# Kernel optimization log

Hardware: AMD Instinct MI355X
Metric: run time of the kernel (lower is better)

Reference implementation:

```python
import jax, jax.numpy as jnp
import numpy as np

B, T, D, H = 4, 1024, 1024, 16
NUM_BUCKETS = 320
MAX_DIST = 800
LN_EPS = 1e-5


def _rel_bucket(T):
    # bidirectional T5-style relative position buckets
    ctx = jnp.arange(T)[:, None]
    mem = jnp.arange(T)[None, :]
    rel = mem - ctx  # (T, T)
    half = NUM_BUCKETS // 2  # 160
    bucket = (rel > 0).astype(jnp.int32) * half
    n = jnp.abs(rel)
    max_exact = half // 2  # 80
    is_small = n < max_exact
    n_f = jnp.maximum(n, 1).astype(jnp.float32)
    large = max_exact + (
        jnp.log(n_f / max_exact) / np.log(MAX_DIST / max_exact) * (half - max_exact)
    ).astype(jnp.int32)
    large = jnp.minimum(large, half - 1)
    return bucket + jnp.where(is_small, n, large)


def setup_inputs() -> dict:
    key = jax.random.key(0)
    ks = jax.random.split(key, 12)
    s = 0.02
    return {
        "x": jax.random.normal(ks[0], (B, T, D), jnp.float32),
        "ln_w": jnp.ones((D,), jnp.float32),
        "ln_b": jnp.zeros((D,), jnp.float32),
        "wq": jax.random.normal(ks[1], (D, D), jnp.float32) * s,
        "bq": jnp.zeros((D,), jnp.float32),
        "wk": jax.random.normal(ks[2], (D, D), jnp.float32) * s,
        "bk": jnp.zeros((D,), jnp.float32),
        "wv": jax.random.normal(ks[3], (D, D), jnp.float32) * s,
        "bv": jnp.zeros((D,), jnp.float32),
        "wo": jax.random.normal(ks[4], (D, D), jnp.float32) * s,
        "bo": jnp.zeros((D,), jnp.float32),
        "rel_emb": jax.random.normal(ks[5], (NUM_BUCKETS, H), jnp.float32) * s,
        "grep_w": jax.random.normal(ks[6], (8, D // H), jnp.float32) * s,
        "grep_b": jnp.zeros((8,), jnp.float32),
        "grep_a": jnp.ones((1, H, 1, 1), jnp.float32),
    }


def reference(x, ln_w, ln_b, wq, bq, wk, bk, wv, bv, wo, bo, rel_emb, grep_w, grep_b, grep_a):
    Bb, Tt, Dd = x.shape
    hd = Dd // H
    scaling = hd ** -0.5
    # pre-norm LayerNorm
    mu = jnp.mean(x, -1, keepdims=True)
    var = jnp.mean((x - mu) ** 2, -1, keepdims=True)
    h = (x - mu) / jnp.sqrt(var + LN_EPS) * ln_w + ln_b
    # projections (q pre-scaled as in fairseq/WavLM)
    q = (h @ wq.T + bq) * scaling
    k = h @ wk.T + bk
    v = h @ wv.T + bv
    q = q.reshape(Bb, Tt, H, hd).transpose(0, 2, 1, 3)  # (B,H,T,hd)
    k = k.reshape(Bb, Tt, H, hd).transpose(0, 2, 1, 3)
    v = v.reshape(Bb, Tt, H, hd).transpose(0, 2, 1, 3)
    # bucketed relative position bias: (H, T, T)
    buckets = _rel_bucket(Tt)
    pos_bias = rel_emb[buckets].transpose(2, 0, 1)
    # gru_rel_pos gating (per batch, head, query position)
    alpha = 32.0
    ql = q * (alpha / scaling)  # undo scaling, multiply by alpha
    g = jax.nn.sigmoid((ql @ grep_w.T + grep_b).reshape(Bb, H, Tt, 2, 4).sum(-1))
    gate_a, gate_b = g[..., 0:1], g[..., 1:2]  # (B,H,T,1)
    gate = gate_a * (gate_b * grep_a - 1.0) + 2.0
    # attention
    scores = jnp.einsum('bhtd,bhsd->bhts', q, k) + gate * pos_bias[None]
    attn = jax.nn.softmax(scores, axis=-1)
    out = jnp.einsum('bhts,bhsd->bhtd', attn, v).transpose(0, 2, 1, 3).reshape(Bb, Tt, Dd)
    # output projection, dropout (identity in eval), residual
    out = out @ wo.T + bo + x
    pos_bias_out = jnp.broadcast_to(pos_bias[None], (Bb, H, Tt, Tt)).reshape(Bb * H, Tt, Tt)
    return out, pos_bias_out
```

## Files before the change

### kernel.cpp

```cpp
#include <hip/hip_runtime.h>

typedef unsigned short u16;
typedef __attribute__((ext_vector_type(8))) short short8;
typedef __attribute__((ext_vector_type(4))) short short4v;
typedef __attribute__((ext_vector_type(4))) float floatx4;

#define MFMA16(a, b, c) __builtin_amdgcn_mfma_f32_16x16x32_bf16(a, b, c, 0, 0, 0)

__device__ __forceinline__ float bf2f(u16 u) {
  return __uint_as_float(((unsigned int)u) << 16);
}
__device__ __forceinline__ u16 f2bf(float f) {
  unsigned int u = __float_as_uint(f);
  unsigned int r = (u + 0x7fffu + ((u >> 16) & 1u)) >> 16;
  return (u16)r;
}
__device__ __forceinline__ void gl_lds16(const u16* g, u16* lds_wave_base) {
  __builtin_amdgcn_global_load_lds(
      (const __attribute__((address_space(1))) unsigned int*)g,
      (__attribute__((address_space(3))) unsigned int*)lds_wave_base, 16, 0, 0);
}

__global__ __launch_bounds__(256) void ln_kernel(
    const float* __restrict__ x, const float* __restrict__ w, const float* __restrict__ bb,
    u16* __restrict__ hb)
{
  int wid = threadIdx.x >> 6, lane = threadIdx.x & 63;
  int row = blockIdx.x * 4 + wid;
  const float* xr = x + row * 1024 + lane * 16;
  float xs[16];
#pragma unroll
  for (int i = 0; i < 4; i++) {
    float4 v = *(const float4*)(xr + i * 4);
    xs[i * 4 + 0] = v.x; xs[i * 4 + 1] = v.y; xs[i * 4 + 2] = v.z; xs[i * 4 + 3] = v.w;
  }
  float s = 0.f, ss = 0.f;
#pragma unroll
  for (int i = 0; i < 16; i++) { s += xs[i]; ss += xs[i] * xs[i]; }
#pragma unroll
  for (int m = 1; m < 64; m <<= 1) { s += __shfl_xor(s, m, 64); ss += __shfl_xor(ss, m, 64); }
  float mu = s * (1.0f / 1024.0f);
  float var = ss * (1.0f / 1024.0f) - mu * mu;
  float rstd = rsqrtf(var + 1e-5f);
  const float* wr = w + lane * 16;
  const float* br = bb + lane * 16;
  short8 o0, o1;
#pragma unroll
  for (int i = 0; i < 8; i++) {
    o0[i] = (short)f2bf((xs[i] - mu) * rstd * wr[i] + br[i]);
    o1[i] = (short)f2bf((xs[8 + i] - mu) * rstd * wr[8 + i] + br[8 + i]);
  }
  u16* hr = hb + row * 1024 + lane * 16;
  *(short8*)hr = o0;
  *(short8*)(hr + 8) = o1;
}

__global__ __launch_bounds__(256) void convw_kernel(
    const float* __restrict__ wq, const float* __restrict__ wk,
    const float* __restrict__ wv, const float* __restrict__ wo,
    u16* __restrict__ wb)
{
  int idx = (blockIdx.x * 256 + threadIdx.x) * 8;
  int seg = idx >> 20, off = idx & 1048575;
  const float* s = (seg == 0) ? wq : (seg == 1) ? wk : (seg == 2) ? wv : wo;
  float4 f0 = *(const float4*)(s + off);
  float4 f1 = *(const float4*)(s + off + 4);
  short8 o;
  o[0] = (short)f2bf(f0.x); o[1] = (short)f2bf(f0.y);
  o[2] = (short)f2bf(f0.z); o[3] = (short)f2bf(f0.w);
  o[4] = (short)f2bf(f1.x); o[5] = (short)f2bf(f1.y);
  o[6] = (short)f2bf(f1.z); o[7] = (short)f2bf(f1.w);
  *(short8*)&wb[idx] = o;
}

__global__ __launch_bounds__(256) void qkv_kernel(
    const u16* __restrict__ hb, const u16* __restrict__ wb,
    const float* __restrict__ bq, const float* __restrict__ bk, const float* __restrict__ bv,
    u16* __restrict__ qs, u16* __restrict__ kko, u16* __restrict__ vt)
{
  __shared__ u16 As[128 * 32];
  __shared__ u16 Bs[128 * 32];
  int tid = threadIdx.x;
  int wid = tid >> 6, lane = tid & 63;
  int wm = wid >> 1, wn = wid & 1;
  int l15 = lane & 15, quad = lane >> 4;
  int m0 = blockIdx.y * 128;
  int n0g = blockIdx.x * 128;
  int sec = n0g >> 10;
  int n0 = n0g & 1023;
  const u16* W = wb + sec * 1048576;
  const float* bias = (sec == 0) ? bq : ((sec == 1) ? bk : bv);

  floatx4 zero4 = {0.f, 0.f, 0.f, 0.f};
  floatx4 acc[4][4];
#pragma unroll
  for (int i = 0; i < 4; i++)
#pragma unroll
    for (int j = 0; j < 4; j++) acc[i][j] = zero4;

  int lr = tid >> 2;
  int lc = (tid & 3) * 8;
  u16* asw = As + wid * 512;
  u16* bsw = Bs + wid * 512;

  for (int kt = 0; kt < 1024; kt += 32) {
    gl_lds16(&hb[(m0 + lr) * 1024 + kt + lc],      asw);
    gl_lds16(&hb[(m0 + lr + 64) * 1024 + kt + lc], asw + 2048);
    gl_lds16(&W[(n0 + lr) * 1024 + kt + lc],       bsw);
    gl_lds16(&W[(n0 + lr + 64) * 1024 + kt + lc],  bsw + 2048);
    __syncthreads();
    short8 af[4], bf[4];
#pragma unroll
    for (int mi = 0; mi < 4; mi++)
      af[mi] = *(const short8*)&As[(wm * 64 + mi * 16 + l15) * 32 + quad * 8];
#pragma unroll
    for (int ni = 0; ni < 4; ni++)
      bf[ni] = *(const short8*)&Bs[(wn * 64 + ni * 16 + l15) * 32 + quad * 8];
#pragma unroll
    for (int mi = 0; mi < 4; mi++)
#pragma unroll
      for (int ni = 0; ni < 4; ni++)
        acc[mi][ni] = MFMA16(af[mi], bf[ni], acc[mi][ni]);
    __syncthreads();
  }

  int bidx = m0 >> 10;
#pragma unroll
  for (int mi = 0; mi < 4; mi++) {
#pragma unroll
    for (int ni = 0; ni < 4; ni++) {
#pragma unroll
      for (int r = 0; r < 4; r++) {
        int row = m0 + wm * 64 + mi * 16 + quad * 4 + r;
        int t = row & 1023;
        int c = n0 + wn * 64 + ni * 16 + l15;
        float val = acc[mi][ni][r] + bias[c];
        int hh = c >> 6, hp = c & 63;
        if (sec == 0) {
          val *= 0.125f;
          qs[((bidx * 16 + hh) * 1024 + t) * 64 + hp] = f2bf(val);
        } else if (sec == 1) {
          kko[((bidx * 16 + hh) * 1024 + t) * 64 + hp] = f2bf(val);
        } else {
          vt[((bidx * 16 + hh) * 64 + hp) * 1024 + t] = f2bf(val);
        }
      }
    }
  }
}

__device__ __forceinline__ int rel_bucket(int t, int s) {
  int rel = s - t;
  int bucket = (rel > 0) ? 160 : 0;
  int n = (rel < 0) ? -rel : rel;
  if (n < 80) return bucket + n;
  float a = logf((float)n / 80.0f);
  float c = a / (float)2.302585092994046;
  float v = c * 80.0f;
  int large = 80 + (int)v;
  if (large > 159) large = 159;
  return bucket + large;
}

__global__ __launch_bounds__(256) void bias0_kernel(
    const float* __restrict__ rel_emb, float* __restrict__ out1,
    u16* __restrict__ bh16, int nb4)
{
  int tid = blockIdx.x * 256 + threadIdx.x;
  int t = tid >> 7;
  int s0 = (tid & 127) * 8;
  int bkt[8], bktT[8];
#pragma unroll
  for (int j = 0; j < 8; j++) {
    bkt[j]  = rel_bucket(t, s0 + j) * 16;
    bktT[j] = rel_bucket(s0 + j, t) * 16;
  }
  int base_ts = t * 1024 + s0;
#pragma unroll
  for (int hh = 0; hh < 16; hh++) {
    float4 v0, v1;
    v0.x = rel_emb[bkt[0] + hh]; v0.y = rel_emb[bkt[1] + hh];
    v0.z = rel_emb[bkt[2] + hh]; v0.w = rel_emb[bkt[3] + hh];
    v1.x = rel_emb[bkt[4] + hh]; v1.y = rel_emb[bkt[5] + hh];
    v1.z = rel_emb[bkt[6] + hh]; v1.w = rel_emb[bkt[7] + hh];
    float* p = out1 + hh * 1048576 + base_ts;
    *(float4*)p = v0;
    *(float4*)(p + 4) = v1;
    if (nb4) {
      *(float4*)(p + 16777216) = v0; *(float4*)(p + 16777216 + 4) = v1;
      *(float4*)(p + 33554432) = v0; *(float4*)(p + 33554432 + 4) = v1;
      *(float4*)(p + 50331648) = v0; *(float4*)(p + 50331648 + 4) = v1;
    }
    short8 o;
#pragma unroll
    for (int j = 0; j < 8; j++) o[j] = (short)f2bf(rel_emb[bktT[j] + hh]);
    *(short8*)(bh16 + hh * 1048576 + base_ts) = o;
  }
}

__global__ __launch_bounds__(256) void bias_copy_kernel(float* __restrict__ out1)
{
  int idx = blockIdx.x * 256 + threadIdx.x;
  float4 v = *(const float4*)&out1[idx * 4];
  *(float4*)&out1[16777216 + idx * 4] = v;
  *(float4*)&out1[33554432 + idx * 4] = v;
  *(float4*)&out1[50331648 + idx * 4] = v;
}

__global__ __launch_bounds__(256, 4) void attn_kernel(
    const u16* __restrict__ qs, const u16* __restrict__ kko, const u16* __restrict__ vt,
    const float* __restrict__ gw, const float* __restrict__ gb, const float* __restrict__ ga,
    const u16* __restrict__ bh16, u16* __restrict__ ao)
{
  __shared__ __align__(16) u16 Pb[4][16 * 72];
  int wid = threadIdx.x >> 6, lane = threadIdx.x & 63;
  int l15 = lane & 15, quad = lane >> 4;
  int bh = blockIdx.x;
  int b = bh >> 4, h = bh & 15;
  int q0 = blockIdx.y * 64 + wid * 16;
  const u16* Q = qs + bh * 65536;
  const u16* K = kko + bh * 65536;
  const u16* V = vt + bh * 65536;
  const u16* BiT = bh16 + h * 1048576;
  u16* pb = &Pb[wid][0];

  const u16* qrow = Q + (q0 + l15) * 64;
  float e[8];
#pragma unroll
  for (int i = 0; i < 8; i++) e[i] = gb[i];
  for (int j = 0; j < 64; j++) {
    float ql = bf2f(qrow[j]) * 256.0f;
#pragma unroll
    for (int i = 0; i < 8; i++) e[i] += ql * gw[i * 64 + j];
  }
  float u0 = e[0] + e[1] + e[2] + e[3];
  float u1 = e[4] + e[5] + e[6] + e[7];
  float sa = 1.0f / (1.0f + __expf(-u0));
  float sb = 1.0f / (1.0f + __expf(-u1));
  float gt = sa * (sb * ga[h] - 1.0f) + 2.0f;

  short8 qf0 = *(const short8*)&Q[(q0 + l15) * 64 + quad * 8];
  short8 qf1 = *(const short8*)&Q[(q0 + l15) * 64 + quad * 8 + 32];
  float mrun = -1e30f, lsum = 0.f;
  floatx4 zero4 = {0.f, 0.f, 0.f, 0.f};
  floatx4 accO[4];
#pragma unroll
  for (int ni = 0; ni < 4; ni++) accO[ni] = zero4;

  for (int s0 = 0; s0 < 1024; s0 += 64) {
    floatx4 sc[4];
#pragma unroll
    for (int tile = 0; tile < 4; tile++) {
      short8 kf = *(const short8*)&K[(s0 + tile * 16 + l15) * 64 + quad * 8];
      sc[tile] = MFMA16(kf, qf0, zero4);
      kf = *(const short8*)&K[(s0 + tile * 16 + l15) * 64 + quad * 8 + 32];
      sc[tile] = MFMA16(kf, qf1, sc[tile]);
    }
    float v[16];
    float mt = -1e30f;
#pragma unroll
    for (int tile = 0; tile < 4; tile++)
#pragma unroll
      for (int r = 0; r < 4; r++) {
        int s = s0 + tile * 16 + quad * 4 + r;
        float val = sc[tile][r] + gt * bf2f(BiT[s * 1024 + q0 + l15]);
        v[tile * 4 + r] = val;
        mt = fmaxf(mt, val);
      }
    mt = fmaxf(mt, __shfl_xor(mt, 16, 64));
    mt = fmaxf(mt, __shfl_xor(mt, 32, 64));
    float mnew = fmaxf(mrun, mt);
    float alpha = __expf(fmaxf(mrun - mnew, -80.0f));
    mrun = mnew;
    float psum = 0.f;
#pragma unroll
    for (int i = 0; i < 16; i++) { v[i] = __expf(v[i] - mnew); psum += v[i]; }
    lsum = lsum * alpha + psum;
#pragma unroll
    for (int ni = 0; ni < 4; ni++) accO[ni] *= alpha;
#pragma unroll
    for (int tile = 0; tile < 4; tile++) {
      short4v o;
#pragma unroll
      for (int r = 0; r < 4; r++) o[r] = (short)f2bf(v[tile * 4 + r]);
      *(short4v*)&pb[l15 * 72 + tile * 16 + quad * 4] = o;
    }
    __asm__ __volatile__("s_waitcnt lgkmcnt(0)" ::: "memory");
    short8 pf0 = *(const short8*)&pb[l15 * 72 + quad * 8];
    short8 pf1 = *(const short8*)&pb[l15 * 72 + 32 + quad * 8];
#pragma unroll
    for (int ni = 0; ni < 4; ni++) {
      short8 vf = *(const short8*)&V[(ni * 16 + l15) * 1024 + s0 + quad * 8];
      accO[ni] = MFMA16(vf, pf0, accO[ni]);
      vf = *(const short8*)&V[(ni * 16 + l15) * 1024 + s0 + 32 + quad * 8];
      accO[ni] = MFMA16(vf, pf1, accO[ni]);
    }
  }
  lsum += __shfl_xor(lsum, 16, 64);
  lsum += __shfl_xor(lsum, 32, 64);
  float linv = 1.0f / lsum;
#pragma unroll
  for (int ni = 0; ni < 4; ni++) {
    short4v o;
#pragma unroll
    for (int r = 0; r < 4; r++) o[r] = (short)f2bf(accO[ni][r] * linv);
    *(short4v*)&pb[l15 * 72 + ni * 16 + quad * 4] = o;
  }
  __asm__ __volatile__("s_waitcnt lgkmcnt(0)" ::: "memory");
#pragma unroll
  for (int r = 0; r < 4; r++) {
    int t = q0 + quad * 4 + r;
#pragma unroll
    for (int ni = 0; ni < 4; ni++) {
      u16 val = pb[(quad * 4 + r) * 72 + ni * 16 + l15];
      ao[(b * 1024 + t) * 1024 + h * 64 + ni * 16 + l15] = val;
    }
  }
}

__global__ __launch_bounds__(256) void oproj_kernel(
    const u16* __restrict__ ao, const u16* __restrict__ wob, const float* __restrict__ bo,
    const float* __restrict__ x, float* __restrict__ out)
{
  __shared__ u16 As[128 * 32];
  __shared__ u16 Bs[128 * 32];
  int tid = threadIdx.x;
  int wid = tid >> 6, lane = tid & 63;
  int wm = wid >> 1, wn = wid & 1;
  int l15 = lane & 15, quad = lane >> 4;
  int m0 = blockIdx.y * 128;
  int n0 = blockIdx.x * 128;

  floatx4 zero4 = {0.f, 0.f, 0.f, 0.f};
  floatx4 acc[4][4];
#pragma unroll
  for (int i = 0; i < 4; i++)
#pragma unroll
    for (int j = 0; j < 4; j++) acc[i][j] = zero4;

  int lr = tid >> 2;
  int lc = (tid & 3) * 8;
  u16* asw = As + wid * 512;
  u16* bsw = Bs + wid * 512;

  for (int kt = 0; kt < 1024; kt += 32) {
    gl_lds16(&ao[(m0 + lr) * 1024 + kt + lc],       asw);
    gl_lds16(&ao[(m0 + lr + 64) * 1024 + kt + lc],  asw + 2048);
    gl_lds16(&wob[(n0 + lr) * 1024 + kt + lc],      bsw);
    gl_lds16(&wob[(n0 + lr + 64) * 1024 + kt + lc], bsw + 2048);
    __syncthreads();
    short8 af[4], bf[4];
#pragma unroll
    for (int mi = 0; mi < 4; mi++)
      af[mi] = *(const short8*)&As[(wm * 64 + mi * 16 + l15) * 32 + quad * 8];
#pragma unroll
    for (int ni = 0; ni < 4; ni++)
      bf[ni] = *(const short8*)&Bs[(wn * 64 + ni * 16 + l15) * 32 + quad * 8];
#pragma unroll
    for (int mi = 0; mi < 4; mi++)
#pragma unroll
      for (int ni = 0; ni < 4; ni++)
        acc[mi][ni] = MFMA16(af[mi], bf[ni], acc[mi][ni]);
    __syncthreads();
  }

#pragma unroll
  for (int mi = 0; mi < 4; mi++) {
#pragma unroll
    for (int ni = 0; ni < 4; ni++) {
#pragma unroll
      for (int r = 0; r < 4; r++) {
        int row = m0 + wm * 64 + mi * 16 + quad * 4 + r;
        int c = n0 + wn * 64 + ni * 16 + l15;
        out[row * 1024 + c] = acc[mi][ni][r] + bo[c] + x[row * 1024 + c];
      }
    }
  }
}

extern "C" void kernel_launch(void* const* d_in, const int* in_sizes, int n_in,
                              void* d_out, int out_size, void* d_ws, size_t ws_size,
                              hipStream_t stream) {
  const float* x    = (const float*)d_in[0];
  const float* ln_w = (const float*)d_in[1];
  const float* ln_b = (const float*)d_in[2];
  const float* wq   = (const float*)d_in[3];
  const float* bq   = (const float*)d_in[4];
  const float* wk   = (const float*)d_in[5];
  const float* bk   = (const float*)d_in[6];
  const float* wv   = (const float*)d_in[7];
  const float* bv   = (const float*)d_in[8];
  const float* wo   = (const float*)d_in[9];
  const float* bo   = (const float*)d_in[10];
  const float* rel  = (const float*)d_in[11];
  const float* gw   = (const float*)d_in[12];
  const float* gb   = (const float*)d_in[13];
  const float* ga   = (const float*)d_in[14];

  float* out0  = (float*)d_out;
  float* out1f = out0 + 4194304;

  int big_ws = (ws_size >= (size_t)(96u << 20)) ? 1 : 0;
  char* sb = big_ws ? (char*)d_ws : (char*)(out1f + 16777216);
  u16* hbb = (u16*)(sb);
  u16* wbb = (u16*)(sb + (8u << 20));
  u16* qsb = (u16*)(sb + (16u << 20));
  u16* kkb = (u16*)(sb + (24u << 20));
  u16* vtb = (u16*)(sb + (32u << 20));
  u16* aob = (u16*)(sb + (40u << 20));
  u16* bhb = (u16*)(sb + (48u << 20));

  ln_kernel<<<1024, 256, 0, stream>>>(x, ln_w, ln_b, hbb);
  convw_kernel<<<2048, 256, 0, stream>>>(wq, wk, wv, wo, wbb);
  qkv_kernel<<<dim3(24, 32), 256, 0, stream>>>(hbb, wbb, bq, bk, bv, qsb, kkb, vtb);
  bias0_kernel<<<512, 256, 0, stream>>>(rel, out1f, bhb, big_ws);
  attn_kernel<<<dim3(64, 16), 256, 0, stream>>>(qsb, kkb, vtb, gw, gb, ga, bhb, aob);
  oproj_kernel<<<dim3(8, 32), 256, 0, stream>>>(aob, wbb + 3145728, bo, x, out0);
  if (!big_ws)
    bias_copy_kernel<<<16384, 256, 0, stream>>>(out1f);
}
```

Measured before the change: 567.7 us.

## Store bias and V in coalesced layouts and vectorize attention bias loads

The bf16 position-bias buffer is now written in row-major (t,s) order, so each attention lane reads four contiguous bf16 values per tile instead of gathering scalars with a 1024-element stride. The QKV epilogue writes V in the same coalesced layout as Q and K, and a new LDS-based transpose kernel produces the transposed V. The gate computation now loads the q row with vector loads, the attention grid is reordered, and the explicit LDS waitcnt barriers are dropped. The costs are an extra kernel launch, an extra read and write of V, and a larger workspace requirement.

Result: no change. 568.8 us (+0.2%).

```diff
diff --git a/kernel.cpp b/kernel.cpp
--- a/kernel.cpp
+++ b/kernel.cpp
@@ -76,7 +76,7 @@
 __global__ __launch_bounds__(256) void qkv_kernel(
     const u16* __restrict__ hb, const u16* __restrict__ wb,
     const float* __restrict__ bq, const float* __restrict__ bk, const float* __restrict__ bv,
-    u16* __restrict__ qs, u16* __restrict__ kko, u16* __restrict__ vt)
+    u16* __restrict__ qs, u16* __restrict__ kko, u16* __restrict__ vraw)
 {
   __shared__ u16 As[128 * 32];
   __shared__ u16 Bs[128 * 32];
@@ -136,17 +136,42 @@
         int c = n0 + wn * 64 + ni * 16 + l15;
         float val = acc[mi][ni][r] + bias[c];
         int hh = c >> 6, hp = c & 63;
+        int addr = ((bidx * 16 + hh) * 1024 + t) * 64 + hp;
         if (sec == 0) {
-          val *= 0.125f;
-          qs[((bidx * 16 + hh) * 1024 + t) * 64 + hp] = f2bf(val);
+          qs[addr] = f2bf(val * 0.125f);
         } else if (sec == 1) {
-          kko[((bidx * 16 + hh) * 1024 + t) * 64 + hp] = f2bf(val);
+          kko[addr] = f2bf(val);
         } else {
-          vt[((bidx * 16 + hh) * 64 + hp) * 1024 + t] = f2bf(val);
+          vraw[addr] = f2bf(val);
         }
       }
     }
   }
+}
+
+__global__ __launch_bounds__(256) void vtrans_kernel(
+    const u16* __restrict__ vraw, u16* __restrict__ vt)
+{
+  __shared__ u16 T[64][72];
+  int bh = blockIdx.y;
+  int t0 = blockIdx.x * 64;
+  const u16* src = vraw + bh * 65536;
+  u16* dst = vt + bh * 65536;
+  int tid = threadIdx.x;
+  int r = tid >> 3;
+  int c8 = (tid & 7) * 8;
+  short8 a = *(const short8*)&src[(t0 + r) * 64 + c8];
+  short8 b = *(const short8*)&src[(t0 + r + 32) * 64 + c8];
+  *(short8*)&T[r][c8] = a;
+  *(short8*)&T[r + 32][c8] = b;
+  __syncthreads();
+  int hd = tid >> 3;
+  int tl = (tid & 7) * 8;
+  short8 o0, o1;
+#pragma unroll
+  for (int j = 0; j < 8; j++) { o0[j] = (short)T[tl + j][hd]; o1[j] = (short)T[tl + j][hd + 32]; }
+  *(short8*)&dst[hd * 1024 + t0 + tl] = o0;
+  *(short8*)&dst[(hd + 32) * 1024 + t0 + tl] = o1;
 }
 
 __device__ __forceinline__ int rel_bucket(int t, int s) {
@@ -169,12 +194,9 @@
   int tid = blockIdx.x * 256 + threadIdx.x;
   int t = tid >> 7;
   int s0 = (tid & 127) * 8;
-  int bkt[8], bktT[8];
-#pragma unroll
-  for (int j = 0; j < 8; j++) {
-    bkt[j]  = rel_bucket(t, s0 + j) * 16;
-    bktT[j] = rel_bucket(s0 + j, t) * 16;
-  }
+  int bkt[8];
+#pragma unroll
+  for (int j = 0; j < 8; j++) bkt[j] = rel_bucket(t, s0 + j) * 16;
   int base_ts = t * 1024 + s0;
 #pragma unroll
   for (int hh = 0; hh < 16; hh++) {
@@ -192,8 +214,10 @@
       *(float4*)(p + 50331648) = v0; *(float4*)(p + 50331648 + 4) = v1;
     }
     short8 o;
-#pragma unroll
-    for (int j = 0; j < 8; j++) o[j] = (short)f2bf(rel_emb[bktT[j] + hh]);
+    o[0] = (short)f2bf(v0.x); o[1] = (short)f2bf(v0.y);
+    o[2] = (short)f2bf(v0.z); o[3] = (short)f2bf(v0.w);
+    o[4] = (short)f2bf(v1.x); o[5] = (short)f2bf(v1.y);
+    o[6] = (short)f2bf(v1.z); o[7] = (short)f2bf(v1.w);
     *(short8*)(bh16 + hh * 1048576 + base_ts) = o;
   }
 }
@@ -215,24 +239,30 @@
   __shared__ __align__(16) u16 Pb[4][16 * 72];
   int wid = threadIdx.x >> 6, lane = threadIdx.x & 63;
   int l15 = lane & 15, quad = lane >> 4;
-  int bh = blockIdx.x;
+  int bh = blockIdx.y;
   int b = bh >> 4, h = bh & 15;
-  int q0 = blockIdx.y * 64 + wid * 16;
+  int q0 = blockIdx.x * 64 + wid * 16;
   const u16* Q = qs + bh * 65536;
   const u16* K = kko + bh * 65536;
   const u16* V = vt + bh * 65536;
-  const u16* BiT = bh16 + h * 1048576;
+  const u16* Bi = bh16 + h * 1048576;
   u16* pb = &Pb[wid][0];
 
   const u16* qrow = Q + (q0 + l15) * 64;
+  short8 q8[8];
+#pragma unroll
+  for (int i = 0; i < 8; i++) q8[i] = *(const short8*)&qrow[i * 8];
   float e[8];
 #pragma unroll
   for (int i = 0; i < 8; i++) e[i] = gb[i];
-  for (int j = 0; j < 64; j++) {
-    float ql = bf2f(qrow[j]) * 256.0f;
-#pragma unroll
-    for (int i = 0; i < 8; i++) e[i] += ql * gw[i * 64 + j];
-  }
+#pragma unroll
+  for (int i8 = 0; i8 < 8; i8++)
+#pragma unroll
+    for (int j = 0; j < 8; j++) {
+      float ql = bf2f((u16)q8[i8][j]) * 256.0f;
+#pragma unroll
+      for (int i = 0; i < 8; i++) e[i] += ql * gw[i * 64 + i8 * 8 + j];
+    }
   float u0 = e[0] + e[1] + e[2] + e[3];
   float u1 = e[4] + e[5] + e[6] + e[7];
   float sa = 1.0f / (1.0f + __expf(-u0));
@@ -248,6 +278,10 @@
   for (int ni = 0; ni < 4; ni++) accO[ni] = zero4;
 
   for (int s0 = 0; s0 < 1024; s0 += 64) {
+    short4v bi4[4];
+#pragma unroll
+    for (int tile = 0; tile < 4; tile++)
+      bi4[tile] = *(const short4v*)&Bi[(q0 + l15) * 1024 + s0 + tile * 16 + quad * 4];
     floatx4 sc[4];
 #pragma unroll
     for (int tile = 0; tile < 4; tile++) {
@@ -262,8 +296,7 @@
     for (int tile = 0; tile < 4; tile++)
 #pragma unroll
       for (int r = 0; r < 4; r++) {
-        int s = s0 + tile * 16 + quad * 4 + r;
-        float val = sc[tile][r] + gt * bf2f(BiT[s * 1024 + q0 + l15]);
+        float val = sc[tile][r] + gt * bf2f((u16)bi4[tile][r]);
         v[tile * 4 + r] = val;
         mt = fmaxf(mt, val);
       }
@@ -285,7 +318,6 @@
       for (int r = 0; r < 4; r++) o[r] = (short)f2bf(v[tile * 4 + r]);
       *(short4v*)&pb[l15 * 72 + tile * 16 + quad * 4] = o;
     }
-    __asm__ __volatile__("s_waitcnt lgkmcnt(0)" ::: "memory");
     short8 pf0 = *(const short8*)&pb[l15 * 72 + quad * 8];
     short8 pf1 = *(const short8*)&pb[l15 * 72 + 32 + quad * 8];
 #pragma unroll
@@ -306,7 +338,6 @@
     for (int r = 0; r < 4; r++) o[r] = (short)f2bf(accO[ni][r] * linv);
     *(short4v*)&pb[l15 * 72 + ni * 16 + quad * 4] = o;
   }
-  __asm__ __volatile__("s_waitcnt lgkmcnt(0)" ::: "memory");
 #pragma unroll
   for (int r = 0; r < 4; r++) {
     int t = q0 + quad * 4 + r;
@@ -400,21 +431,23 @@
   float* out0  = (float*)d_out;
   float* out1f = out0 + 4194304;
 
-  int big_ws = (ws_size >= (size_t)(96u << 20)) ? 1 : 0;
+  int big_ws = (ws_size >= (size_t)(128u << 20)) ? 1 : 0;
   char* sb = big_ws ? (char*)d_ws : (char*)(out1f + 16777216);
-  u16* hbb = (u16*)(sb);
-  u16* wbb = (u16*)(sb + (8u << 20));
-  u16* qsb = (u16*)(sb + (16u << 20));
-  u16* kkb = (u16*)(sb + (24u << 20));
-  u16* vtb = (u16*)(sb + (32u << 20));
-  u16* aob = (u16*)(sb + (40u << 20));
-  u16* bhb = (u16*)(sb + (48u << 20));
+  u16* hbb  = (u16*)(sb);
+  u16* wbb  = (u16*)(sb + (8u << 20));
+  u16* qsb  = (u16*)(sb + (16u << 20));
+  u16* kkb  = (u16*)(sb + (24u << 20));
+  u16* vtb  = (u16*)(sb + (32u << 20));
+  u16* aob  = (u16*)(sb + (40u << 20));
+  u16* bhb  = (u16*)(sb + (48u << 20));
+  u16* vrw  = (u16*)(sb + (80u << 20));
 
   ln_kernel<<<1024, 256, 0, stream>>>(x, ln_w, ln_b, hbb);
   convw_kernel<<<2048, 256, 0, stream>>>(wq, wk, wv, wo, wbb);
-  qkv_kernel<<<dim3(24, 32), 256, 0, stream>>>(hbb, wbb, bq, bk, bv, qsb, kkb, vtb);
+  qkv_kernel<<<dim3(24, 32), 256, 0, stream>>>(hbb, wbb, bq, bk, bv, qsb, kkb, vrw);
+  vtrans_kernel<<<dim3(16, 64), 256, 0, stream>>>(vrw, vtb);
   bias0_kernel<<<512, 256, 0, stream>>>(rel, out1f, bhb, big_ws);
-  attn_kernel<<<dim3(64, 16), 256, 0, stream>>>(qsb, kkb, vtb, gw, gb, ga, bhb, aob);
+  attn_kernel<<<dim3(16, 64), 256, 0, stream>>>(qsb, kkb, vtb, gw, gb, ga, bhb, aob);
   oproj_kernel<<<dim3(8, 32), 256, 0, stream>>>(aob, wbb + 3145728, bo, x, out0);
   if (!big_ws)
     bias_copy_kernel<<<16384, 256, 0, stream>>>(out1f);
```
